# Performance work log

Hardware: AMD Instinct MI355X
Metric: run time of the kernel (lower is better)

The kernel has to match this reference:

```python
import jax, jax.numpy as jnp
import numpy as np
import math

NUM_HEADS = 16
ROPE_BASE = 10000.0


def _rope_cos_sin(seq_len, head_dim, dtype):
    # Qwen2-style rotary embeddings. The torch source builds cos/sin of width
    # head_dim by concatenating freqs with itself, so the first and second
    # halves are identical; the half-width table below is the equivalent math.
    half = head_dim // 2
    inv_freq = 1.0 / (ROPE_BASE ** (jnp.arange(0, head_dim, 2, dtype=jnp.float32) / head_dim))
    t = jnp.arange(seq_len, dtype=jnp.float32)
    freqs = jnp.einsum('i,j->ij', t, inv_freq)  # [S, half]
    cos = jnp.cos(freqs).astype(dtype)[None, None]  # [1,1,S,half]
    sin = jnp.sin(freqs).astype(dtype)[None, None]
    return cos, sin


def _apply_rope(x, cos, sin):
    # x: [B, H, S, D]; split-half rotation (Qwen2 rotate-half convention)
    half = x.shape[-1] // 2
    x1, x2 = x[..., :half], x[..., half:]
    return jnp.concatenate([x1 * cos - x2 * sin, x2 * cos + x1 * sin], axis=-1)


def setup_inputs() -> dict:
    key = jax.random.key(0)
    ks = jax.random.split(key, 5)
    B, S, H = 2, 2048, 2048
    scale = 1.0 / math.sqrt(H)
    return {
        'hidden_states': jax.random.normal(ks[0], (B, S, H), dtype=jnp.float32),
        'Wq': jax.random.normal(ks[1], (H, H), dtype=jnp.float32) * scale,
        'Wk': jax.random.normal(ks[2], (H, H), dtype=jnp.float32) * scale,
        'Wv': jax.random.normal(ks[3], (H, H), dtype=jnp.float32) * scale,
        'Wo': jax.random.normal(ks[4], (H, H), dtype=jnp.float32) * scale,
    }


def reference(hidden_states, Wq, Wk, Wv, Wo):
    B, S, H = hidden_states.shape
    nh = NUM_HEADS
    hd = H // nh

    def proj(W):
        # nn.Linear: x @ W.T ; then [B,S,H] -> [B,nh,S,hd]
        y = jnp.einsum('bsh,oh->bso', hidden_states, W)
        return y.reshape(B, S, nh, hd).transpose(0, 2, 1, 3)

    q, k, v = proj(Wq), proj(Wk), proj(Wv)

    cos, sin = _rope_cos_sin(S, hd, hidden_states.dtype)
    q = _apply_rope(q, cos, sin)
    k = _apply_rope(k, cos, sin)

    scores = jnp.einsum('bhqd,bhkd->bhqk', q, k) / math.sqrt(hd)
    causal = jnp.triu(jnp.full((S, S), -jnp.inf, dtype=scores.dtype), k=1)
    scores = scores + causal[None, None]
    probs = jax.nn.softmax(scores, axis=-1)

    ctx = jnp.einsum('bhqk,bhkd->bhqd', probs, v)  # [B,nh,S,hd]
    ctx = ctx.transpose(0, 2, 1, 3).reshape(B, S, H)
    out = jnp.einsum('bsh,oh->bso', ctx, Wo)
    return out
```

## Files before the change

kernel.cpp:

```cpp
#include <hip/hip_runtime.h>

#define S_LEN 2048
#define HID   2048
#define NHEAD 16
#define HD    128
#define BSZ   2
#define BS_TOT (BSZ * S_LEN)

typedef __bf16 bf16x8 __attribute__((ext_vector_type(8)));
typedef unsigned short u16x8 __attribute__((ext_vector_type(8)));
typedef unsigned short u16x4 __attribute__((ext_vector_type(4)));
typedef float f32x4 __attribute__((ext_vector_type(4)));

static __device__ __forceinline__ bf16x8 as_bf(u16x8 v) { return __builtin_bit_cast(bf16x8, v); }

static __device__ __forceinline__ unsigned short f2bf(float f) {
  unsigned int u = __builtin_bit_cast(unsigned int, f);
  u += 0x7fffu + ((u >> 16) & 1u);
  return (unsigned short)(u >> 16);
}
static __device__ __forceinline__ float bf2f(unsigned short b) {
  unsigned int u = ((unsigned int)b) << 16;
  return __builtin_bit_cast(float, u);
}

__global__ __launch_bounds__(256) void cvt_bf16(const float* __restrict__ in,
                                                unsigned short* __restrict__ out) {
  int i = blockIdx.x * 256 + threadIdx.x;
  float4 v = ((const float4*)in)[i];
  ushort4 o;
  o.x = f2bf(v.x); o.y = f2bf(v.y); o.z = f2bf(v.z); o.w = f2bf(v.w);
  ((ushort4*)out)[i] = o;
}

__global__ __launch_bounds__(256) void rope_table(float* __restrict__ ct, float* __restrict__ st) {
  int id = blockIdx.x * 256 + threadIdx.x;
  int t = id >> 6, d = id & 63;
  float inv = powf(10000.0f, -(float)d * (1.0f / 64.0f));
  float f = (float)t * inv;
  float sv, cv;
  sincosf(f, &sv, &cv);
  ct[id] = cv; st[id] = sv;
}

__global__ __launch_bounds__(256) void rope_apply(unsigned short* __restrict__ q,
                                                  unsigned short* __restrict__ k,
                                                  const float* __restrict__ ct,
                                                  const float* __restrict__ st) {
  int id = blockIdx.x * 256 + threadIdx.x;
  int d = id & 63;
  int h = (id >> 6) & (NHEAD - 1);
  int m = id >> 10;
  int s = m & (S_LEN - 1);
  float c = ct[s * 64 + d], sn = st[s * 64 + d];
  size_t base = (size_t)m * HID + h * HD + d;
  float q1 = bf2f(q[base]), q2 = bf2f(q[base + 64]);
  q[base]      = f2bf(q1 * c - q2 * sn);
  q[base + 64] = f2bf(q2 * c + q1 * sn);
  float k1 = bf2f(k[base]), k2 = bf2f(k[base + 64]);
  k[base]      = f2bf(k1 * c - k2 * sn);
  k[base + 64] = f2bf(k2 * c + k1 * sn);
}

template <typename OutT>
__global__ __launch_bounds__(256) void gemm_bt(const unsigned short* __restrict__ A,
                                               const unsigned short* __restrict__ Bw,
                                               OutT* __restrict__ C, int M, int N, int K) {
  __shared__ __align__(16) unsigned short As[128 * 32];
  __shared__ __align__(16) unsigned short Bs[128 * 32];
  const int nbn = N >> 7;
  int bm = blockIdx.x / nbn, bn = blockIdx.x % nbn;
  int tid = (int)threadIdx.x;
  int l = tid & 63, lr = l & 15, lg = l >> 4;
  int w = tid >> 6, wm = w >> 1, wn = w & 1;

  int rA0 = tid >> 2, c8 = tid & 3;
  size_t gA0 = (size_t)(bm * 128 + rA0) * K + c8 * 8;
  size_t gB0 = (size_t)(bn * 128 + rA0) * K + c8 * 8;
  int ws0 = rA0 * 32 + ((c8 ^ (rA0 & 3)) << 3);
  int ws1 = ws0 + 64 * 32;

  int aoff[4], boff[4];
#pragma unroll
  for (int i = 0; i < 4; ++i) {
    int rowa = wm * 64 + i * 16 + lr;
    aoff[i] = rowa * 32 + ((lg ^ (rowa & 3)) << 3);
    int rowb = wn * 64 + i * 16 + lr;
    boff[i] = rowb * 32 + ((lg ^ (rowb & 3)) << 3);
  }

  f32x4 zero = {0.f, 0.f, 0.f, 0.f};
  f32x4 acc[4][4];
#pragma unroll
  for (int mi = 0; mi < 4; ++mi)
#pragma unroll
    for (int ni = 0; ni < 4; ++ni) acc[mi][ni] = zero;

  int nk = K >> 5;
  u16x8 ra0 = *(const u16x8*)(A + gA0);
  u16x8 ra1 = *(const u16x8*)(A + gA0 + (size_t)64 * K);
  u16x8 rb0 = *(const u16x8*)(Bw + gB0);
  u16x8 rb1 = *(const u16x8*)(Bw + gB0 + (size_t)64 * K);

  for (int kt = 0; kt < nk; ++kt) {
    __syncthreads();
    *(u16x8*)&As[ws0] = ra0; *(u16x8*)&As[ws1] = ra1;
    *(u16x8*)&Bs[ws0] = rb0; *(u16x8*)&Bs[ws1] = rb1;
    __syncthreads();
    if (kt + 1 < nk) {
      size_t kadd = (size_t)(kt + 1) * 32;
      ra0 = *(const u16x8*)(A + gA0 + kadd);
      ra1 = *(const u16x8*)(A + gA0 + (size_t)64 * K + kadd);
      rb0 = *(const u16x8*)(Bw + gB0 + kadd);
      rb1 = *(const u16x8*)(Bw + gB0 + (size_t)64 * K + kadd);
    }
    u16x8 af[4], bfr[4];
#pragma unroll
    for (int i = 0; i < 4; ++i) {
      af[i]  = *(const u16x8*)&As[aoff[i]];
      bfr[i] = *(const u16x8*)&Bs[boff[i]];
    }
#pragma unroll
    for (int mi = 0; mi < 4; ++mi)
#pragma unroll
      for (int ni = 0; ni < 4; ++ni)
        acc[mi][ni] = __builtin_amdgcn_mfma_f32_16x16x32_bf16(as_bf(af[mi]), as_bf(bfr[ni]),
                                                              acc[mi][ni], 0, 0, 0);
  }

#pragma unroll
  for (int mi = 0; mi < 4; ++mi) {
#pragma unroll
    for (int ni = 0; ni < 4; ++ni) {
      int col = bn * 128 + wn * 64 + ni * 16 + lr;
#pragma unroll
      for (int j = 0; j < 4; ++j) {
        int rowm = bm * 128 + wm * 64 + mi * 16 + 4 * lg + j;
        float v = acc[mi][ni][j];
        if constexpr (sizeof(OutT) == 2) C[(size_t)rowm * N + col] = f2bf(v);
        else                             C[(size_t)rowm * N + col] = v;
      }
    }
  }
}

__global__ __launch_bounds__(256, 2) void attn_fwd(const unsigned short* __restrict__ qg,
                                                   const unsigned short* __restrict__ kg,
                                                   const unsigned short* __restrict__ vt,
                                                   unsigned short* __restrict__ ctx) {
  __shared__ __align__(16) unsigned short Ks[64 * 128];
  __shared__ __align__(16) unsigned short Vs[128 * 64];
  __shared__ __align__(16) unsigned short Ps[4 * 32 * 64];

  int x = (int)blockIdx.x;
  int bh = (x & 7) * 4 + ((x >> 3) & 3);
  int qt = 15 - (x >> 5);
  int b = bh >> 4, h = bh & 15;
  int q0 = qt * 128;
  int nt = 2 * qt + 2;

  int tid = (int)threadIdx.x;
  int w = tid >> 6, l = tid & 63, lr = l & 15, lg = l >> 4;
  const float scale = 0.08838834764831845f;
  const int bS = b * S_LEN, h128 = h * HD;
  const int qw = q0 + w * 32;

  u16x8 qfr[2][4];
#pragma unroll
  for (int qf = 0; qf < 2; ++qf) {
    const unsigned short* qb = qg + (size_t)(bS + qw + qf * 16 + lr) * HID + h128;
#pragma unroll
    for (int kk = 0; kk < 4; ++kk) qfr[qf][kk] = *(const u16x8*)(qb + kk * 32 + lg * 8);
  }

  f32x4 zero = {0.f, 0.f, 0.f, 0.f};
  f32x4 oacc[2][8];
#pragma unroll
  for (int qf = 0; qf < 2; ++qf)
#pragma unroll
    for (int nj = 0; nj < 8; ++nj) oacc[qf][nj] = zero;
  float mrow[2] = {-1e30f, -1e30f}, lsum[2] = {0.f, 0.f};

  int rK[4], cK[4], dV[4], cV[4];
#pragma unroll
  for (int p = 0; p < 4; ++p) {
    int id = tid + p * 256;
    rK[p] = id >> 4; cK[p] = id & 15;
    dV[p] = id >> 3; cV[p] = id & 7;
  }

  u16x8 ka[4], va[4];
#pragma unroll
  for (int p = 0; p < 4; ++p) {
    ka[p] = *(const u16x8*)(kg + (size_t)(bS + rK[p]) * HID + h128 + cK[p] * 8);
    va[p] = *(const u16x8*)(vt + (size_t)(h128 + dV[p]) * BS_TOT + bS + cV[p] * 8);
  }

  for (int t = 0; t < nt; ++t) {
    int k0 = t * 64;
    __syncthreads();
#pragma unroll
    for (int p = 0; p < 4; ++p) {
      *(u16x8*)&Ks[rK[p] * 128 + ((cK[p] ^ (rK[p] & 15)) * 8)] = ka[p];
      *(u16x8*)&Vs[dV[p] * 64 + ((cV[p] ^ (dV[p] & 7)) * 8)] = va[p];
    }
    __syncthreads();
    if (t + 1 < nt) {
      int k1 = k0 + 64;
#pragma unroll
      for (int p = 0; p < 4; ++p) {
        ka[p] = *(const u16x8*)(kg + (size_t)(bS + k1 + rK[p]) * HID + h128 + cK[p] * 8);
        va[p] = *(const u16x8*)(vt + (size_t)(h128 + dV[p]) * BS_TOT + bS + k1 + cV[p] * 8);
      }
    }

    if (k0 <= qw + 31) {
      f32x4 sac[2][4];
#pragma unroll
      for (int qf = 0; qf < 2; ++qf)
#pragma unroll
        for (int ni = 0; ni < 4; ++ni) sac[qf][ni] = zero;
#pragma unroll
      for (int kk = 0; kk < 4; ++kk) {
#pragma unroll
        for (int ni = 0; ni < 4; ++ni) {
          u16x8 kf = *(const u16x8*)&Ks[(ni * 16 + lr) * 128 + (((kk * 4 + lg) ^ lr) * 8)];
          sac[0][ni] = __builtin_amdgcn_mfma_f32_16x16x32_bf16(as_bf(kf), as_bf(qfr[0][kk]), sac[0][ni], 0, 0, 0);
          sac[1][ni] = __builtin_amdgcn_mfma_f32_16x16x32_bf16(as_bf(kf), as_bf(qfr[1][kk]), sac[1][ni], 0, 0, 0);
        }
      }
      bool needmask = (k0 + 63 > qw);

#pragma unroll
      for (int qf = 0; qf < 2; ++qf) {
        float s[4][4];
#pragma unroll
        for (int ni = 0; ni < 4; ++ni)
#pragma unroll
          for (int j = 0; j < 4; ++j) s[ni][j] = sac[qf][ni][j] * scale;
        if (needmask) {
          int qgl = qw + qf * 16 + lr;
#pragma unroll
          for (int ni = 0; ni < 4; ++ni)
#pragma unroll
            for (int j = 0; j < 4; ++j)
              if (k0 + ni * 16 + 4 * lg + j > qgl) s[ni][j] = -1e30f;
        }
        float mx = s[0][0];
#pragma unroll
        for (int ni = 0; ni < 4; ++ni)
#pragma unroll
          for (int j = 0; j < 4; ++j) mx = fmaxf(mx, s[ni][j]);
        mx = fmaxf(mx, __shfl_xor(mx, 16));
        mx = fmaxf(mx, __shfl_xor(mx, 32));
        float mn = fmaxf(mrow[qf], mx);
        float al = __expf(mrow[qf] - mn);
        mrow[qf] = mn;
        float rs = 0.f;
#pragma unroll
        for (int ni = 0; ni < 4; ++ni)
#pragma unroll
          for (int j = 0; j < 4; ++j) { float p = __expf(s[ni][j] - mn); s[ni][j] = p; rs += p; }
        rs += __shfl_xor(rs, 16);
        rs += __shfl_xor(rs, 32);
        lsum[qf] = lsum[qf] * al + rs;
        float a0 = __shfl(al, 4 * lg + 0, 16);
        float a1 = __shfl(al, 4 * lg + 1, 16);
        float a2 = __shfl(al, 4 * lg + 2, 16);
        float a3 = __shfl(al, 4 * lg + 3, 16);
#pragma unroll
        for (int nj = 0; nj < 8; ++nj) {
          oacc[qf][nj][0] *= a0; oacc[qf][nj][1] *= a1;
          oacc[qf][nj][2] *= a2; oacc[qf][nj][3] *= a3;
        }
        unsigned short* pw = &Ps[w * 2048];
#pragma unroll
        for (int ni = 0; ni < 4; ++ni) {
          u16x4 pv = {f2bf(s[ni][0]), f2bf(s[ni][1]), f2bf(s[ni][2]), f2bf(s[ni][3])};
          *(u16x4*)&pw[(qf * 16 + lr) * 64 + (((2 * ni + (lg >> 1)) ^ (lr & 7)) * 8) + (lg & 1) * 4] = pv;
        }
      }

      const unsigned short* pw = &Ps[w * 2048];
#pragma unroll
      for (int kk2 = 0; kk2 < 2; ++kk2) {
        u16x8 pa0 = *(const u16x8*)&pw[(0 * 16 + lr) * 64 + (((kk2 * 4 + lg) ^ (lr & 7)) * 8)];
        u16x8 pa1 = *(const u16x8*)&pw[(1 * 16 + lr) * 64 + (((kk2 * 4 + lg) ^ (lr & 7)) * 8)];
#pragma unroll
        for (int nj = 0; nj < 8; ++nj) {
          u16x8 vf = *(const u16x8*)&Vs[(nj * 16 + lr) * 64 + (((kk2 * 4 + lg) ^ (lr & 7)) * 8)];
          oacc[0][nj] = __builtin_amdgcn_mfma_f32_16x16x32_bf16(as_bf(pa0), as_bf(vf), oacc[0][nj], 0, 0, 0);
          oacc[1][nj] = __builtin_amdgcn_mfma_f32_16x16x32_bf16(as_bf(pa1), as_bf(vf), oacc[1][nj], 0, 0, 0);
        }
      }
    }
  }

#pragma unroll
  for (int qf = 0; qf < 2; ++qf) {
    float rl = 1.0f / lsum[qf];
    float r0 = __shfl(rl, 4 * lg + 0, 16);
    float r1 = __shfl(rl, 4 * lg + 1, 16);
    float r2 = __shfl(rl, 4 * lg + 2, 16);
    float r3 = __shfl(rl, 4 * lg + 3, 16);
    size_t obase = (size_t)(bS + qw + qf * 16 + 4 * lg) * HID + h128;
#pragma unroll
    for (int nj = 0; nj < 8; ++nj) {
      ctx[obase + 0 * HID + nj * 16 + lr] = f2bf(oacc[qf][nj][0] * r0);
      ctx[obase + 1 * HID + nj * 16 + lr] = f2bf(oacc[qf][nj][1] * r1);
      ctx[obase + 2 * HID + nj * 16 + lr] = f2bf(oacc[qf][nj][2] * r2);
      ctx[obase + 3 * HID + nj * 16 + lr] = f2bf(oacc[qf][nj][3] * r3);
    }
  }
}

extern "C" void kernel_launch(void* const* d_in, const int* in_sizes, int n_in,
                              void* d_out, int out_size, void* d_ws, size_t ws_size,
                              hipStream_t stream) {
  const float* hs = (const float*)d_in[0];
  const float* Wq = (const float*)d_in[1];
  const float* Wk = (const float*)d_in[2];
  const float* Wv = (const float*)d_in[3];
  const float* Wo = (const float*)d_in[4];

  char* ws = (char*)d_ws;
  unsigned short* hsb = (unsigned short*)(ws);
  unsigned short* wqb = (unsigned short*)(ws + 16777216);
  unsigned short* wkb = (unsigned short*)(ws + 25165824);
  unsigned short* wvb = (unsigned short*)(ws + 33554432);
  unsigned short* wob = (unsigned short*)(ws + 41943040);
  unsigned short* qb  = (unsigned short*)(ws + 50331648);
  unsigned short* kb  = (unsigned short*)(ws + 67108864);
  unsigned short* vtb = (unsigned short*)(ws + 83886080);
  float* ctab = (float*)(ws + 100663296);
  float* stab = (float*)(ws + 101187584);
  unsigned short* ctxb = hsb;

  cvt_bf16<<<8192, 256, 0, stream>>>(hs, hsb);
  cvt_bf16<<<4096, 256, 0, stream>>>(Wq, wqb);
  cvt_bf16<<<4096, 256, 0, stream>>>(Wk, wkb);
  cvt_bf16<<<4096, 256, 0, stream>>>(Wv, wvb);
  cvt_bf16<<<4096, 256, 0, stream>>>(Wo, wob);
  rope_table<<<512, 256, 0, stream>>>(ctab, stab);

  gemm_bt<unsigned short><<<512, 256, 0, stream>>>(hsb, wqb, qb, BS_TOT, HID, HID);
  gemm_bt<unsigned short><<<512, 256, 0, stream>>>(hsb, wkb, kb, BS_TOT, HID, HID);
  gemm_bt<unsigned short><<<512, 256, 0, stream>>>(wvb, hsb, vtb, HID, BS_TOT, HID);

  rope_apply<<<16384, 256, 0, stream>>>(qb, kb, ctab, stab);

  attn_fwd<<<512, 256, 0, stream>>>(qb, kb, vtb, ctxb);

  gemm_bt<float><<<512, 256, 0, stream>>>(ctxb, wob, (float*)d_out, BS_TOT, HID, HID);

  (void)in_sizes; (void)n_in; (void)out_size; (void)ws_size;
}
```

Measured before the change: 298.9 us.

## Use direct global-to-LDS loads in GEMM and lazy-rescale softmax in attention

The GEMM staging now uses global_load_lds so global data goes straight into shared memory, with no register round trip and no LDS swizzle. The price is that the register prefetch overlap is gone and bank conflicts may appear. The attention kernel folds the scale into an exp2 constant and only rescales the accumulator when the row max grows past a threshold, defers the row-sum shuffle reduction to the epilogue, and changes the block-to-tile ordering. f2bf switches to the compiler's native bf16 conversion.

```diff
diff --git a/kernel.cpp b/kernel.cpp
--- a/kernel.cpp
+++ b/kernel.cpp
@@ -15,13 +15,17 @@
 static __device__ __forceinline__ bf16x8 as_bf(u16x8 v) { return __builtin_bit_cast(bf16x8, v); }
 
 static __device__ __forceinline__ unsigned short f2bf(float f) {
-  unsigned int u = __builtin_bit_cast(unsigned int, f);
-  u += 0x7fffu + ((u >> 16) & 1u);
-  return (unsigned short)(u >> 16);
+  __bf16 h = (__bf16)f;
+  return __builtin_bit_cast(unsigned short, h);
 }
 static __device__ __forceinline__ float bf2f(unsigned short b) {
   unsigned int u = ((unsigned int)b) << 16;
   return __builtin_bit_cast(float, u);
+}
+
+static __device__ __forceinline__ void gload_lds16(const unsigned short* g, unsigned short* l) {
+  __builtin_amdgcn_global_load_lds((const __attribute__((address_space(1))) unsigned int*)g,
+                                   (__attribute__((address_space(3))) unsigned int*)l, 16, 0, 0);
 }
 
 __global__ __launch_bounds__(256) void cvt_bf16(const float* __restrict__ in,
@@ -74,19 +78,17 @@
   int l = tid & 63, lr = l & 15, lg = l >> 4;
   int w = tid >> 6, wm = w >> 1, wn = w & 1;
 
-  int rA0 = tid >> 2, c8 = tid & 3;
-  size_t gA0 = (size_t)(bm * 128 + rA0) * K + c8 * 8;
-  size_t gB0 = (size_t)(bn * 128 + rA0) * K + c8 * 8;
-  int ws0 = rA0 * 32 + ((c8 ^ (rA0 & 3)) << 3);
-  int ws1 = ws0 + 64 * 32;
+  int srow = 32 * w + (l >> 2);
+  const unsigned short* gA = A + (size_t)(bm * 128 + srow) * K + (l & 3) * 8;
+  const unsigned short* gB = Bw + (size_t)(bn * 128 + srow) * K + (l & 3) * 8;
+  unsigned short* lA = &As[(32 * w) * 32];
+  unsigned short* lB = &Bs[(32 * w) * 32];
 
   int aoff[4], boff[4];
 #pragma unroll
   for (int i = 0; i < 4; ++i) {
-    int rowa = wm * 64 + i * 16 + lr;
-    aoff[i] = rowa * 32 + ((lg ^ (rowa & 3)) << 3);
-    int rowb = wn * 64 + i * 16 + lr;
-    boff[i] = rowb * 32 + ((lg ^ (rowb & 3)) << 3);
+    aoff[i] = (wm * 64 + i * 16 + lr) * 32 + lg * 8;
+    boff[i] = (wn * 64 + i * 16 + lr) * 32 + lg * 8;
   }
 
   f32x4 zero = {0.f, 0.f, 0.f, 0.f};
@@ -97,23 +99,16 @@
     for (int ni = 0; ni < 4; ++ni) acc[mi][ni] = zero;
 
   int nk = K >> 5;
-  u16x8 ra0 = *(const u16x8*)(A + gA0);
-  u16x8 ra1 = *(const u16x8*)(A + gA0 + (size_t)64 * K);
-  u16x8 rb0 = *(const u16x8*)(Bw + gB0);
-  u16x8 rb1 = *(const u16x8*)(Bw + gB0 + (size_t)64 * K);
-
   for (int kt = 0; kt < nk; ++kt) {
     __syncthreads();
-    *(u16x8*)&As[ws0] = ra0; *(u16x8*)&As[ws1] = ra1;
-    *(u16x8*)&Bs[ws0] = rb0; *(u16x8*)&Bs[ws1] = rb1;
+    const unsigned short* pa = gA + kt * 32;
+    const unsigned short* pb = gB + kt * 32;
+    gload_lds16(pa, lA);
+    gload_lds16(pa + (size_t)16 * K, lA + 16 * 32);
+    gload_lds16(pb, lB);
+    gload_lds16(pb + (size_t)16 * K, lB + 16 * 32);
     __syncthreads();
-    if (kt + 1 < nk) {
-      size_t kadd = (size_t)(kt + 1) * 32;
-      ra0 = *(const u16x8*)(A + gA0 + kadd);
-      ra1 = *(const u16x8*)(A + gA0 + (size_t)64 * K + kadd);
-      rb0 = *(const u16x8*)(Bw + gB0 + kadd);
-      rb1 = *(const u16x8*)(Bw + gB0 + (size_t)64 * K + kadd);
-    }
+
     u16x8 af[4], bfr[4];
 #pragma unroll
     for (int i = 0; i < 4; ++i) {
@@ -142,6 +137,7 @@
       }
     }
   }
+  (void)M;
 }
 
 __global__ __launch_bounds__(256, 2) void attn_fwd(const unsigned short* __restrict__ qg,
@@ -153,15 +149,17 @@
   __shared__ __align__(16) unsigned short Ps[4 * 32 * 64];
 
   int x = (int)blockIdx.x;
-  int bh = (x & 7) * 4 + ((x >> 3) & 3);
-  int qt = 15 - (x >> 5);
+  int bh, qt;
+  if (x < 256) { bh = x & 31;         qt = 15 - (x >> 5); }
+  else         { bh = (x - 256) & 31; qt = (x - 256) >> 5; }
   int b = bh >> 4, h = bh & 15;
   int q0 = qt * 128;
   int nt = 2 * qt + 2;
 
   int tid = (int)threadIdx.x;
   int w = tid >> 6, l = tid & 63, lr = l & 15, lg = l >> 4;
-  const float scale = 0.08838834764831845f;
+  const float CEXP = 0.12751744f;
+  const float THRRAW = 90.509668f;
   const int bS = b * S_LEN, h128 = h * HD;
   const int qw = q0 + w * 32;
 
@@ -237,7 +235,7 @@
 #pragma unroll
         for (int ni = 0; ni < 4; ++ni)
 #pragma unroll
-          for (int j = 0; j < 4; ++j) s[ni][j] = sac[qf][ni][j] * scale;
+          for (int j = 0; j < 4; ++j) s[ni][j] = sac[qf][ni][j];
         if (needmask) {
           int qgl = qw + qf * 16 + lr;
 #pragma unroll
@@ -253,26 +251,31 @@
           for (int j = 0; j < 4; ++j) mx = fmaxf(mx, s[ni][j]);
         mx = fmaxf(mx, __shfl_xor(mx, 16));
         mx = fmaxf(mx, __shfl_xor(mx, 32));
-        float mn = fmaxf(mrow[qf], mx);
-        float al = __expf(mrow[qf] - mn);
-        mrow[qf] = mn;
+        if (!__all(mx - mrow[qf] <= THRRAW)) {
+          float mn = fmaxf(mrow[qf], mx);
+          float al = exp2f((mrow[qf] - mn) * CEXP);
+          mrow[qf] = mn;
+          lsum[qf] *= al;
+          float a0 = __shfl(al, 4 * lg + 0, 16);
+          float a1 = __shfl(al, 4 * lg + 1, 16);
+          float a2 = __shfl(al, 4 * lg + 2, 16);
+          float a3 = __shfl(al, 4 * lg + 3, 16);
+#pragma unroll
+          for (int nj = 0; nj < 8; ++nj) {
+            oacc[qf][nj][0] *= a0; oacc[qf][nj][1] *= a1;
+            oacc[qf][nj][2] *= a2; oacc[qf][nj][3] *= a3;
+          }
+        }
+        float m = mrow[qf];
         float rs = 0.f;
 #pragma unroll
         for (int ni = 0; ni < 4; ++ni)
 #pragma unroll
-          for (int j = 0; j < 4; ++j) { float p = __expf(s[ni][j] - mn); s[ni][j] = p; rs += p; }
-        rs += __shfl_xor(rs, 16);
-        rs += __shfl_xor(rs, 32);
-        lsum[qf] = lsum[qf] * al + rs;
-        float a0 = __shfl(al, 4 * lg + 0, 16);
-        float a1 = __shfl(al, 4 * lg + 1, 16);
-        float a2 = __shfl(al, 4 * lg + 2, 16);
-        float a3 = __shfl(al, 4 * lg + 3, 16);
-#pragma unroll
-        for (int nj = 0; nj < 8; ++nj) {
-          oacc[qf][nj][0] *= a0; oacc[qf][nj][1] *= a1;
-          oacc[qf][nj][2] *= a2; oacc[qf][nj][3] *= a3;
-        }
+          for (int j = 0; j < 4; ++j) {
+            float p = exp2f((s[ni][j] - m) * CEXP);
+            s[ni][j] = p; rs += p;
+          }
+        lsum[qf] += rs;
         unsigned short* pw = &Ps[w * 2048];
 #pragma unroll
         for (int ni = 0; ni < 4; ++ni) {
@@ -298,7 +301,10 @@
 
 #pragma unroll
   for (int qf = 0; qf < 2; ++qf) {
-    float rl = 1.0f / lsum[qf];
+    float ls = lsum[qf];
+    ls += __shfl_xor(ls, 16);
+    ls += __shfl_xor(ls, 32);
+    float rl = 1.0f / ls;
     float r0 = __shfl(rl, 4 * lg + 0, 16);
     float r1 = __shfl(rl, 4 * lg + 1, 16);
     float r2 = __shfl(rl, 4 * lg + 2, 16);
```

Result: slower. 331.7 us (+11.0%).
